# Kernel tuning notes

Hardware: AMD Instinct MI355X
Metric: run time of the kernel (lower is better)

The kernel has to match this reference:

```python
import jax, jax.numpy as jnp
import numpy as np

E = 8        # num_experts
K = 2        # top_k routing
D = 1024     # d_model
F = 4096     # expert hidden (ffn) dim
EPS = 1e-5


def _layernorm(h, g, b):
    # h: [E, T, C]; g, b: [E, C]
    mu = h.mean(axis=-1, keepdims=True)
    var = ((h - mu) ** 2).mean(axis=-1, keepdims=True)
    return (h - mu) * jax.lax.rsqrt(var + EPS) * g[:, None, :] + b[:, None, :]


def setup_inputs() -> dict:
    key = jax.random.key(0)
    ks = jax.random.split(key, 8)
    B, S = 2, 2048
    x = jax.random.normal(ks[0], (B, S, D), dtype=jnp.float32)
    Wr = jax.random.normal(ks[1], (D, E), dtype=jnp.float32) / np.sqrt(D)
    br = jnp.zeros((E,), dtype=jnp.float32)
    W1 = jax.random.normal(ks[2], (E, D, F), dtype=jnp.float32) / np.sqrt(D)
    b1 = jnp.zeros((E, F), dtype=jnp.float32)
    g1 = jnp.ones((E, F), dtype=jnp.float32)
    be1 = jnp.zeros((E, F), dtype=jnp.float32)
    W2 = jax.random.normal(ks[3], (E, F, D), dtype=jnp.float32) / np.sqrt(F)
    b2 = jnp.zeros((E, D), dtype=jnp.float32)
    g2 = jnp.ones((E, D), dtype=jnp.float32)
    be2 = jnp.zeros((E, D), dtype=jnp.float32)
    return {"x": x, "Wr": Wr, "br": br, "W1": W1, "b1": b1, "g1": g1,
            "be1": be1, "W2": W2, "b2": b2, "g2": g2, "be2": be2}


def reference(x, Wr, br, W1, b1, g1, be1, W2, b2, g2, be2):
    B, S, _ = x.shape
    xt = x.reshape(-1, D)                       # [T, D] token matrix
    # --- router + sampler: top-k softmax probs, renormalized over the k slots
    logits = xt @ Wr + br                       # [T, E]
    p = jax.nn.softmax(logits, axis=-1)
    probs, idx = jax.lax.top_k(p, K)            # [T, K]
    probs = probs / probs.sum(axis=-1, keepdims=True)
    # --- experts layer 1: Linear -> relu -> LayerNorm, per expert
    h = jnp.einsum('td,edf->etf', xt, W1) + b1[:, None, :]   # [E, T, F]
    h = _layernorm(jax.nn.relu(h), g1, be1)
    # --- experts layer 2: Linear -> relu -> LayerNorm
    y = jnp.einsum('etf,efd->etd', h, W2) + b2[:, None, :]   # [E, T, D]
    y = _layernorm(jax.nn.relu(y), g2, be2)
    # --- weighted scatter-combine: gate[t,e] = sum_k 1[idx[t,k]==e] * probs[t,k]
    gate = (jax.nn.one_hot(idx, E, dtype=x.dtype) * probs[..., None]).sum(axis=1)  # [T, E]
    out = jnp.einsum('te,etd->td', gate, y)     # index_add combine, dense form
    return out.reshape(B, S, D)
```

## Files before the change

### kernel.cpp

```cpp
#include <hip/hip_runtime.h>


#define E_N 8
#define TOPK 2
#define DM 1024
#define FF 4096
#define NTOK 4096
#define NA 8192
#define LN_EPS 1e-5f
#define NBX 128

typedef __attribute__((ext_vector_type(4))) float f32x4;
typedef __attribute__((ext_vector_type(8))) short short8;

__device__ __forceinline__ unsigned short f2bf(float f) {
    unsigned int u = __builtin_bit_cast(unsigned int, f);
    u = (u + 0x7FFFu + ((u >> 16) & 1u)) >> 16;
    return (unsigned short)u;
}
__device__ __forceinline__ float bf2f(unsigned short h) {
    unsigned int u = ((unsigned int)h) << 16;
    return __builtin_bit_cast(float, u);
}
__device__ __forceinline__ void unp(unsigned int u, float& lo, float& hi) {
    lo = bf2f((unsigned short)(u & 0xffffu));
    hi = bf2f((unsigned short)(u >> 16));
}
__device__ __forceinline__ unsigned int pk(float lo, float hi) {
    return (unsigned int)f2bf(lo) | ((unsigned int)f2bf(hi) << 16);
}

__device__ __forceinline__ void gload16(const unsigned short* g, unsigned short* lds) {
    __builtin_amdgcn_global_load_lds(
        (const __attribute__((address_space(1))) unsigned int*)g,
        (__attribute__((address_space(3))) unsigned int*)lds, 16, 0, 0);
}

__device__ __forceinline__ void make_btile(const float* __restrict__ s, int sld,
                                           unsigned short* __restrict__ out,
                                           float* tile) {
    int tid = threadIdx.x;
    int wv = tid >> 6, lane = tid & 63;
    int kl = lane >> 5;
    int n = (lane & 31) * 4;
#pragma unroll
    for (int i = 0; i < 8; i++) {
        int j = wv * 8 + i;
        int k = j * 2 + kl;
        gload16((const unsigned short*)(s + (size_t)k * sld + n),
                (unsigned short*)(tile + j * 256));
    }
    __syncthreads();
    int r = tid >> 1, gh = (tid & 1) * 4;
    const float* col = tile + r;
    unsigned int ov[16];
#pragma unroll
    for (int i = 0; i < 4; i++) {
        int kb = ((gh + i) ^ (r & 7)) << 3;
#pragma unroll
        for (int ee = 0; ee < 8; ee += 2)
            ov[i * 4 + (ee >> 1)] = pk(col[(kb + ee) * 128], col[(kb + ee + 1) * 128]);
    }
    unsigned short* dp = out + (size_t)r * 64 + gh * 8;
#pragma unroll
    for (int i = 0; i < 4; i++)
        *(uint4*)(dp + i * 8) = *(uint4*)&ov[i * 4];
}


__global__ __launch_bounds__(256) void k_prep(
        const float* __restrict__ W1, const float* __restrict__ W2,
        unsigned short* __restrict__ W1T, unsigned short* __restrict__ W2T,
        const float* __restrict__ x, const float* __restrict__ Wr,
        const float* __restrict__ br, unsigned short* __restrict__ xb,
        int* __restrict__ topk_idx, float* __restrict__ topk_p)
{
    __shared__ float tile[64 * 128];
    int bid = blockIdx.x;
    int tid = threadIdx.x;

    if (bid >= 8192) {
        int blk = bid - 8192;
        int wv = tid >> 6, lane = tid & 63;
        int t = blk * 4 + wv;
        const float* xr = x + (size_t)t * DM;
        unsigned short* xbr = xb + (size_t)t * DM;
        float4 xv[4];
#pragma unroll
        for (int p = 0; p < 4; p++)
            xv[p] = *(const float4*)(xr + p * 256 + lane * 4);
#pragma unroll
        for (int p = 0; p < 4; p++) {
            uint2 pkd; pkd.x = pk(xv[p].x, xv[p].y); pkd.y = pk(xv[p].z, xv[p].w);
            *(uint2*)(xbr + p * 256 + lane * 4) = pkd;
        }
        float a0=0,a1=0,a2=0,a3=0,a4=0,a5=0,a6=0,a7=0;
#pragma unroll
        for (int p = 0; p < 4; p++) {
            int d0 = p * 256 + lane * 4;
            float xs[4] = {xv[p].x, xv[p].y, xv[p].z, xv[p].w};
#pragma unroll
            for (int j = 0; j < 4; j++) {
                const float4* wp = (const float4*)(Wr + (d0 + j) * 8);
                float4 w0 = wp[0], w1 = wp[1];
                a0 += xs[j] * w0.x; a1 += xs[j] * w0.y; a2 += xs[j] * w0.z; a3 += xs[j] * w0.w;
                a4 += xs[j] * w1.x; a5 += xs[j] * w1.y; a6 += xs[j] * w1.z; a7 += xs[j] * w1.w;
            }
        }
#pragma unroll
        for (int off = 32; off; off >>= 1) {
            a0 += __shfl_xor(a0, off); a1 += __shfl_xor(a1, off);
            a2 += __shfl_xor(a2, off); a3 += __shfl_xor(a3, off);
            a4 += __shfl_xor(a4, off); a5 += __shfl_xor(a5, off);
            a6 += __shfl_xor(a6, off); a7 += __shfl_xor(a7, off);
        }
        if (lane == 0) {
            float l[8] = {a0 + br[0], a1 + br[1], a2 + br[2], a3 + br[3],
                          a4 + br[4], a5 + br[5], a6 + br[6], a7 + br[7]};
            int i0 = 0;
#pragma unroll
            for (int e = 1; e < 8; e++) if (l[e] > l[i0]) i0 = e;
            int i1 = (i0 == 0) ? 1 : 0;
#pragma unroll
            for (int e = 0; e < 8; e++) if (e != i0 && l[e] > l[i1]) i1 = e;
            float p1 = expf(l[i1] - l[i0]);
            float s = 1.0f + p1;
            topk_idx[2 * t]     = i0;
            topk_idx[2 * t + 1] = i1;
            topk_p[2 * t]       = 1.0f / s;
            topk_p[2 * t + 1]   = p1 / s;
        }
        return;
    }

    if (bid < 4096) {
        int z = bid >> 9, nt = (bid >> 4) & 31, kt = bid & 15;
        make_btile(W1 + (size_t)z * DM * FF + (size_t)(kt * 64) * FF + nt * 128, FF,
                   W1T + (((size_t)z * 32 + nt) * 16 + kt) * 8192, tile);
    } else {
        int b = bid - 4096;
        int e = b >> 9, nt = (b >> 6) & 7, kt = b & 63;
        make_btile(W2 + (size_t)e * FF * DM + (size_t)(kt * 64) * DM + nt * 128, DM,
                   W2T + (((size_t)e * 8 + nt) * 64 + kt) * 8192, tile);
    }
}


__global__ __launch_bounds__(256) void k_route2(const int* __restrict__ topk_idx,
        int* __restrict__ cnt, int* __restrict__ offs,
        int* __restrict__ assign_tok, int* __restrict__ assign_e,
        int* __restrict__ slot)
{
    __shared__ int h[8], base[8];
    int tid = threadIdx.x;
    if (tid < 8) h[tid] = 0;
    __syncthreads();
    int el[32];
#pragma unroll
    for (int i = 0; i < 32; i++) {
        int idx = tid * 32 + i;
        el[i] = topk_idx[idx];
        atomicAdd(&h[el[i]], 1);
    }
    __syncthreads();
    if (tid == 0) {
        int s = 0;
        for (int e = 0; e < E_N; e++) { offs[e] = s; cnt[e] = h[e]; base[e] = s; s += h[e]; }
        offs[E_N] = s;
    }
    __syncthreads();
    if (tid < 8) h[tid] = base[tid];
    __syncthreads();
#pragma unroll
    for (int i = 0; i < 32; i++) {
        int idx = tid * 32 + i;
        int e = el[i];
        int pos = atomicAdd(&h[e], 1);
        assign_tok[pos] = idx >> 1;
        assign_e[pos] = e;
        slot[idx] = pos;
    }
}


template<bool GATHER, bool EPI>
__global__ __launch_bounds__(256, 4) void k_gemm(
    const unsigned short* __restrict__ A,
    const unsigned short* __restrict__ BT,
    const float* __restrict__ bias,
    unsigned short* __restrict__ C,
    const int* __restrict__ cnt, const int* __restrict__ offs,
    const int* __restrict__ gather_tok,
    int Kslice, int N, int ldA, int NT, int KT, int GX, int KS, size_t slicePitch)
{
    __shared__ __align__(1024) char lds[32768];

    int bid = blockIdx.x;
    int e = bid & 7;
    int lb = bid >> 3;
    int M = cnt[e];
    if (M <= 0) return;
    int off_e = offs[e];
    int nrows = (M + 127) >> 7;
    int ntiles = nrows * GX * KS;

    int tid = threadIdx.x;
    int wv = tid >> 6, lane = tid & 63;
    int lr = lane & 15, hi = lane >> 4;
    int mW = (wv >> 1) * 64, nW = (wv & 1) * 64;
    int colsw = ((lane & 7) ^ (lane >> 3)) * 8;
    int l3 = lane >> 3;
    int nt = Kslice >> 6;

    for (int t = lb; t < ntiles; t += NBX) {
        int r = t % nrows;
        int q = t / nrows;
        int xn = q % GX;
        int ks = q / GX;
        int m0 = r * 128;
        int n0 = xn * 128;
        int kbase = ks * Kslice;

        const unsigned short* aptr[4];
        const unsigned short* bptr[4];
        size_t btile = ((size_t)(e * NT + xn) * KT + (size_t)ks * nt) * 8192;
#pragma unroll
        for (int i = 0; i < 4; i++) {
            int j = wv * 4 + i;
            int rr = m0 + j * 8 + l3; rr = (rr < M) ? rr : (M - 1);
            size_t arow = GATHER ? (size_t)gather_tok[off_e + rr] : (size_t)(off_e + rr);
            aptr[i] = A + arow * (size_t)ldA + kbase + colsw;
            bptr[i] = BT + btile + j * 512 + lane * 8;
        }

        f32x4 acc[4][4];
        f32x4 zz = {0.f, 0.f, 0.f, 0.f};
#pragma unroll
        for (int mi = 0; mi < 4; mi++)
#pragma unroll
            for (int ni = 0; ni < 4; ni++) acc[mi][ni] = zz;

        for (int kt = 0; kt < nt; ++kt) {
            __syncthreads();
#pragma unroll
            for (int i = 0; i < 4; i++) {
                gload16(aptr[i] + kt * 64, (unsigned short*)(lds + (wv * 4 + i) * 1024));
                gload16(bptr[i] + (size_t)kt * 8192,
                        (unsigned short*)(lds + 16384 + (wv * 4 + i) * 1024));
            }
            __syncthreads();
#pragma unroll
            for (int kss = 0; kss < 2; kss++) {
                int cb = (kss * 64 + hi * 16) ^ ((lr & 7) << 4);
                short8 afr[4], bfr[4];
#pragma unroll
                for (int ni = 0; ni < 4; ni++)
                    bfr[ni] = *(const short8*)(lds + 16384 + (nW + ni * 16 + lr) * 128 + cb);
#pragma unroll
                for (int mi = 0; mi < 4; mi++)
                    afr[mi] = *(const short8*)(lds + (mW + mi * 16 + lr) * 128 + cb);
                __builtin_amdgcn_s_setprio(1);
#pragma unroll
                for (int mi = 0; mi < 4; mi++)
#pragma unroll
                    for (int ni = 0; ni < 4; ni++)
                        acc[mi][ni] = __builtin_amdgcn_mfma_f32_16x16x32_bf16(
                            afr[mi], bfr[ni], acc[mi][ni], 0, 0, 0);
                __builtin_amdgcn_s_setprio(0);
            }
        }

        unsigned short* Cs = C + ks * slicePitch;
        float bv[4] = {0.f, 0.f, 0.f, 0.f};
        if (EPI) {
#pragma unroll
            for (int ni = 0; ni < 4; ni++)
                bv[ni] = bias[(size_t)e * N + (n0 + nW + ni * 16 + lr)];
        }
#pragma unroll
        for (int mi = 0; mi < 4; mi++) {
            int mb = m0 + mW + mi * 16 + hi * 4;
#pragma unroll
            for (int rr = 0; rr < 4; rr++) {
                int m = mb + rr;
                if (m < M) {
                    unsigned short* crow = Cs + (size_t)(off_e + m) * N;
#pragma unroll
                    for (int ni = 0; ni < 4; ni++) {
                        float v = acc[mi][ni][rr];
                        if (EPI) v = fmaxf(v + bv[ni], 0.0f);
                        crow[n0 + nW + ni * 16 + lr] = f2bf(v);
                    }
                }
            }
        }
    }
}


__global__ __launch_bounds__(256) void k_ln1(unsigned short* __restrict__ H,
        const float* __restrict__ g, const float* __restrict__ b,
        const int* __restrict__ assign_e)
{
    size_t a = blockIdx.x;
    int e = assign_e[a];
    unsigned short* row = H + a * FF;
    int tid = threadIdx.x;
    uint4 u0 = *(const uint4*)(row + tid * 16);
    uint4 u1 = *(const uint4*)(row + tid * 16 + 8);
    float v[16];
    unp(u0.x, v[0], v[1]);  unp(u0.y, v[2], v[3]);
    unp(u0.z, v[4], v[5]);  unp(u0.w, v[6], v[7]);
    unp(u1.x, v[8], v[9]);  unp(u1.y, v[10], v[11]);
    unp(u1.z, v[12], v[13]); unp(u1.w, v[14], v[15]);
    float s = 0.f, q = 0.f;
#pragma unroll
    for (int i = 0; i < 16; i++) { s += v[i]; q += v[i] * v[i]; }
#pragma unroll
    for (int off = 32; off; off >>= 1) { s += __shfl_xor(s, off); q += __shfl_xor(q, off); }
    __shared__ float red[8];
    int wv = tid >> 6, lane = tid & 63;
    if (lane == 0) { red[wv * 2] = s; red[wv * 2 + 1] = q; }
    __syncthreads();
    s = red[0] + red[2] + red[4] + red[6];
    q = red[1] + red[3] + red[5] + red[7];
    float mu = s * (1.0f / FF);
    float var = q * (1.0f / FF) - mu * mu;
    float rstd = rsqrtf(var + LN_EPS);
    const float* gg = g + (size_t)e * FF + tid * 16;
    const float* bb = b + (size_t)e * FF + tid * 16;
    float4 G0 = *(const float4*)(gg);      float4 G1 = *(const float4*)(gg + 4);
    float4 G2 = *(const float4*)(gg + 8);  float4 G3 = *(const float4*)(gg + 12);
    float4 B0 = *(const float4*)(bb);      float4 B1 = *(const float4*)(bb + 4);
    float4 B2 = *(const float4*)(bb + 8);  float4 B3 = *(const float4*)(bb + 12);
    float gvv[16] = {G0.x,G0.y,G0.z,G0.w,G1.x,G1.y,G1.z,G1.w,G2.x,G2.y,G2.z,G2.w,G3.x,G3.y,G3.z,G3.w};
    float bvv[16] = {B0.x,B0.y,B0.z,B0.w,B1.x,B1.y,B1.z,B1.w,B2.x,B2.y,B2.z,B2.w,B3.x,B3.y,B3.z,B3.w};
#pragma unroll
    for (int i = 0; i < 16; i++) v[i] = (v[i] - mu) * rstd * gvv[i] + bvv[i];
    u0.x = pk(v[0], v[1]);  u0.y = pk(v[2], v[3]);
    u0.z = pk(v[4], v[5]);  u0.w = pk(v[6], v[7]);
    u1.x = pk(v[8], v[9]);  u1.y = pk(v[10], v[11]);
    u1.z = pk(v[12], v[13]); u1.w = pk(v[14], v[15]);
    *(uint4*)(row + tid * 16) = u0;
    *(uint4*)(row + tid * 16 + 8) = u1;
}


__global__ __launch_bounds__(256) void k_comb(const unsigned short* __restrict__ Yp,
        const float* __restrict__ g, const float* __restrict__ b2,
        const float* __restrict__ be,
        const int* __restrict__ slot, const float* __restrict__ topk_p,
        const int* __restrict__ assign_e, float* __restrict__ out)
{
    int t = blockIdx.x;
    int s0 = slot[2 * t], s1 = slot[2 * t + 1];
    float p0 = topk_p[2 * t], p1 = topk_p[2 * t + 1];
    int e0 = assign_e[s0], e1 = assign_e[s1];
    int tid = threadIdx.x;
    int d = tid * 4;
    const unsigned short* Y1 = Yp + (size_t)NA * DM;
    uint2 ua0 = *(const uint2*)(Yp + (size_t)s0 * DM + d);
    uint2 ua1 = *(const uint2*)(Y1 + (size_t)s0 * DM + d);
    uint2 ub0 = *(const uint2*)(Yp + (size_t)s1 * DM + d);
    uint2 ub1 = *(const uint2*)(Y1 + (size_t)s1 * DM + d);
    float4 bza = *(const float4*)(b2 + (size_t)e0 * DM + d);
    float4 bzb = *(const float4*)(b2 + (size_t)e1 * DM + d);
    float x0, x1, y0, y1;
    float va[4], vb[4];
    unp(ua0.x, x0, x1); unp(ua1.x, y0, y1);
    va[0] = fmaxf(x0 + y0 + bza.x, 0.f); va[1] = fmaxf(x1 + y1 + bza.y, 0.f);
    unp(ua0.y, x0, x1); unp(ua1.y, y0, y1);
    va[2] = fmaxf(x0 + y0 + bza.z, 0.f); va[3] = fmaxf(x1 + y1 + bza.w, 0.f);
    unp(ub0.x, x0, x1); unp(ub1.x, y0, y1);
    vb[0] = fmaxf(x0 + y0 + bzb.x, 0.f); vb[1] = fmaxf(x1 + y1 + bzb.y, 0.f);
    unp(ub0.y, x0, x1); unp(ub1.y, y0, y1);
    vb[2] = fmaxf(x0 + y0 + bzb.z, 0.f); vb[3] = fmaxf(x1 + y1 + bzb.w, 0.f);

    float sa = 0.f, qa = 0.f, sb = 0.f, qb = 0.f;
#pragma unroll
    for (int i = 0; i < 4; i++) {
        sa += va[i]; qa += va[i] * va[i];
        sb += vb[i]; qb += vb[i] * vb[i];
    }
#pragma unroll
    for (int off = 32; off; off >>= 1) {
        sa += __shfl_xor(sa, off); qa += __shfl_xor(qa, off);
        sb += __shfl_xor(sb, off); qb += __shfl_xor(qb, off);
    }
    __shared__ float red[16];
    int wv = tid >> 6, lane = tid & 63;
    if (lane == 0) { red[wv*4+0]=sa; red[wv*4+1]=qa; red[wv*4+2]=sb; red[wv*4+3]=qb; }
    __syncthreads();
    sa = red[0] + red[4] + red[8]  + red[12];
    qa = red[1] + red[5] + red[9]  + red[13];
    sb = red[2] + red[6] + red[10] + red[14];
    qb = red[3] + red[7] + red[11] + red[15];
    float mua = sa * (1.0f / DM), vara = qa * (1.0f / DM) - mua * mua;
    float ra = rsqrtf(vara + LN_EPS);
    float mub = sb * (1.0f / DM), varb = qb * (1.0f / DM) - mub * mub;
    float rb = rsqrtf(varb + LN_EPS);
    float4 ga  = *(const float4*)(g + (size_t)e0 * DM + d);
    float4 ba  = *(const float4*)(be + (size_t)e0 * DM + d);
    float4 gb4 = *(const float4*)(g + (size_t)e1 * DM + d);
    float4 bb4 = *(const float4*)(be + (size_t)e1 * DM + d);
    float4 o;
    o.x = p0 * ((va[0] - mua) * ra * ga.x + ba.x) + p1 * ((vb[0] - mub) * rb * gb4.x + bb4.x);
    o.y = p0 * ((va[1] - mua) * ra * ga.y + ba.y) + p1 * ((vb[1] - mub) * rb * gb4.y + bb4.y);
    o.z = p0 * ((va[2] - mua) * ra * ga.z + ba.z) + p1 * ((vb[2] - mub) * rb * gb4.z + bb4.z);
    o.w = p0 * ((va[3] - mua) * ra * ga.w + ba.w) + p1 * ((vb[3] - mub) * rb * gb4.w + bb4.w);
    *(float4*)(out + (size_t)t * DM + d) = o;
}


extern "C" void kernel_launch(void* const* d_in, const int* in_sizes, int n_in,
                              void* d_out, int out_size, void* d_ws, size_t ws_size,
                              hipStream_t stream) {
    const float* x   = (const float*)d_in[0];
    const float* Wr  = (const float*)d_in[1];
    const float* br  = (const float*)d_in[2];
    const float* W1  = (const float*)d_in[3];
    const float* b1  = (const float*)d_in[4];
    const float* g1  = (const float*)d_in[5];
    const float* be1 = (const float*)d_in[6];
    const float* W2  = (const float*)d_in[7];
    const float* b2  = (const float*)d_in[8];
    const float* g2  = (const float*)d_in[9];
    const float* be2 = (const float*)d_in[10];
    float* out = (float*)d_out;

    char* w = (char*)d_ws;
    int*   cnt        = (int*)(w);
    int*   offs       = (int*)(w + 128);
    int*   topk_idx   = (int*)(w + 512);
    float* topk_p     = (float*)(w + 512 + (32 << 10));
    int*   assign_tok = (int*)(w + 512 + (64 << 10));
    int*   assign_e   = (int*)(w + 512 + (96 << 10));
    int*   slot       = (int*)(w + 512 + (128 << 10));
    unsigned short* xb  = (unsigned short*)(w + ((size_t)1 << 20));
    unsigned short* W1T = (unsigned short*)(w + ((size_t)9 << 20));
    unsigned short* W2T = (unsigned short*)(w + ((size_t)73 << 20));
    unsigned short* Hb  = (unsigned short*)(w + ((size_t)137 << 20));
    unsigned short* Yp  = (unsigned short*)(w + ((size_t)201 << 20));

    k_prep<<<9216, 256, 0, stream>>>(
        W1, W2, W1T, W2T, x, Wr, br, xb, topk_idx, topk_p);
    k_route2<<<1, 256, 0, stream>>>(topk_idx, cnt, offs, assign_tok, assign_e, slot);
    k_gemm<true, true><<<8 * NBX, 256, 0, stream>>>(
        xb, W1T, b1, Hb, cnt, offs, assign_tok, DM, FF, DM, 32, 16, 32, 1, 0);
    k_ln1<<<NA, 256, 0, stream>>>(Hb, g1, be1, assign_e);
    k_gemm<false, false><<<8 * NBX, 256, 0, stream>>>(
        Hb, W2T, nullptr, Yp, cnt, offs, nullptr, FF / 2, DM, FF, 8, 64, 8, 2,
        (size_t)NA * DM);
    k_comb<<<NTOK, 256, 0, stream>>>(Yp, g2, b2, be2, slot, topk_p, assign_e, out);
}
```

Baseline: 332.3 us.

## Double-buffer weight-tile conversion in k_prep, four tiles per block

Each weight-conversion block in k_prep now processes four consecutive K tiles instead of one. It uses two LDS buffers so the async global-to-LDS load of the next tile overlaps the bf16 pack and store of the current tile. The grid shrinks accordingly, and the router blocks start at a new block offset. The aim is to hide load latency and cut per-block launch overhead in this memory-bound fp32-to-bf16 weight transpose. In exchange, LDS use per block doubles, which may lower the number of resident blocks per CU.

```diff
diff --git a/kernel.cpp b/kernel.cpp
--- a/kernel.cpp
+++ b/kernel.cpp
@@ -36,9 +36,8 @@
         (__attribute__((address_space(3))) unsigned int*)lds, 16, 0, 0);
 }
 
-__device__ __forceinline__ void make_btile(const float* __restrict__ s, int sld,
-                                           unsigned short* __restrict__ out,
-                                           float* tile) {
+__device__ __forceinline__ void stage_tile(const float* __restrict__ s, int sld,
+                                           float* buf) {
     int tid = threadIdx.x;
     int wv = tid >> 6, lane = tid & 63;
     int kl = lane >> 5;
@@ -48,9 +47,13 @@
         int j = wv * 8 + i;
         int k = j * 2 + kl;
         gload16((const unsigned short*)(s + (size_t)k * sld + n),
-                (unsigned short*)(tile + j * 256));
-    }
-    __syncthreads();
+                (unsigned short*)(buf + j * 256));
+    }
+}
+
+__device__ __forceinline__ void emit_tile(const float* __restrict__ tile,
+                                          unsigned short* __restrict__ out) {
+    int tid = threadIdx.x;
     int r = tid >> 1, gh = (tid & 1) * 4;
     const float* col = tile + r;
     unsigned int ov[16];
@@ -75,12 +78,12 @@
         const float* __restrict__ br, unsigned short* __restrict__ xb,
         int* __restrict__ topk_idx, float* __restrict__ topk_p)
 {
-    __shared__ float tile[64 * 128];
+    __shared__ float tile[2][64 * 128];
     int bid = blockIdx.x;
     int tid = threadIdx.x;
 
-    if (bid >= 8192) {
-        int blk = bid - 8192;
+    if (bid >= 2048) {
+        int blk = bid - 2048;
         int wv = tid >> 6, lane = tid & 63;
         int t = blk * 4 + wv;
         const float* xr = x + (size_t)t * DM;
@@ -133,15 +136,28 @@
         return;
     }
 
-    if (bid < 4096) {
-        int z = bid >> 9, nt = (bid >> 4) & 31, kt = bid & 15;
-        make_btile(W1 + (size_t)z * DM * FF + (size_t)(kt * 64) * FF + nt * 128, FF,
-                   W1T + (((size_t)z * 32 + nt) * 16 + kt) * 8192, tile);
+    const float* s; unsigned short* o; int sld;
+    if (bid < 1024) {
+        int z = bid >> 7, nt = (bid >> 2) & 31, kt0 = (bid & 3) * 4;
+        s = W1 + (size_t)z * DM * FF + (size_t)(kt0 * 64) * FF + nt * 128;
+        sld = FF;
+        o = W1T + (((size_t)z * 32 + nt) * 16 + kt0) * 8192;
     } else {
-        int b = bid - 4096;
-        int e = b >> 9, nt = (b >> 6) & 7, kt = b & 63;
-        make_btile(W2 + (size_t)e * FF * DM + (size_t)(kt * 64) * DM + nt * 128, DM,
-                   W2T + (((size_t)e * 8 + nt) * 64 + kt) * 8192, tile);
+        int b = bid - 1024;
+        int e = b >> 7, nt = (b >> 4) & 7, kt0 = (b & 15) * 4;
+        s = W2 + (size_t)e * FF * DM + (size_t)(kt0 * 64) * DM + nt * 128;
+        sld = DM;
+        o = W2T + (((size_t)e * 8 + nt) * 64 + kt0) * 8192;
+    }
+
+    stage_tile(s, sld, tile[0]);
+    __syncthreads();
+#pragma unroll
+    for (int q = 0; q < 4; q++) {
+        if (q < 3)
+            stage_tile(s + (size_t)(q + 1) * 64 * sld, sld, tile[(q + 1) & 1]);
+        emit_tile(tile[q & 1], o + (size_t)q * 8192);
+        if (q < 3) __syncthreads();
     }
 }
 
@@ -442,7 +458,7 @@
     unsigned short* Hb  = (unsigned short*)(w + ((size_t)137 << 20));
     unsigned short* Yp  = (unsigned short*)(w + ((size_t)201 << 20));
 
-    k_prep<<<9216, 256, 0, stream>>>(
+    k_prep<<<3072, 256, 0, stream>>>(
         W1, W2, W1T, W2T, x, Wr, br, xb, topk_idx, topk_p);
     k_route2<<<1, 256, 0, stream>>>(topk_idx, cnt, offs, assign_tok, assign_e, slot);
     k_gemm<true, true><<<8 * NBX, 256, 0, stream>>>(
```

Result: no change. 333.4 us (+0.3%).
